# Performance work log

Measured on AMD Instinct MI355X. Metric: run time of the kernel, lower is better.

## Reference

```python
import jax, jax.numpy as jnp
import numpy as np

GRID_SIZE = 5
SPLINE_ORDER = 3
EPS = 1e-5


def make_grid(in_features):
    # efficient-kan: grid_range=[-1,1], points from -order..grid_size+order
    h = 2.0 / GRID_SIZE
    g = jnp.arange(-SPLINE_ORDER, GRID_SIZE + SPLINE_ORDER + 1, dtype=jnp.float32) * h - 1.0
    return jnp.tile(g[None, :], (in_features, 1))  # [in, grid_size + 2*order + 1]


def b_splines(x, grid):
    # x: [B, in], grid: [in, G] -> bases: [B, in, grid_size + order]
    xg = x[:, :, None]
    bases = ((xg >= grid[:, :-1]) & (xg < grid[:, 1:])).astype(x.dtype)
    for k in range(1, SPLINE_ORDER + 1):
        left = (xg - grid[:, : -(k + 1)]) / (grid[:, k:-1] - grid[:, : -(k + 1)])
        right = (grid[:, k + 1:] - xg) / (grid[:, k + 1:] - grid[:, 1:-k])
        bases = left * bases[:, :, :-1] + right * bases[:, :, 1:]
    return bases


def kan_linear(x, grid, base_w, spline_w, spline_scaler):
    # base path: silu(x) @ base_w.T ; spline path: bsplines(x) contracted with scaled spline weight
    base_out = jnp.einsum('bi,oi->bo', jax.nn.silu(x), base_w)
    bases = b_splines(x, grid)  # [B, in, C]
    sw = spline_w * spline_scaler[:, :, None]  # [out, in, C]
    spline_out = jnp.einsum('bic,oic->bo', bases, sw)
    return base_out + spline_out


def layer_norm(x, w, b):
    mu = jnp.mean(x, axis=-1, keepdims=True)
    var = jnp.mean(jnp.square(x - mu), axis=-1, keepdims=True)
    return (x - mu) * jax.lax.rsqrt(var + EPS) * w + b


def setup_inputs() -> dict:
    key = jax.random.key(0)
    ks = jax.random.split(key, 8)
    B, F, H, E = 65536, 32, 64, 64
    OUT = E * F  # 2048
    C = GRID_SIZE + SPLINE_ORDER  # 8 coeffs per edge
    x = jax.random.normal(ks[0], (B, F), dtype=jnp.float32)
    return {
        'x': x,
        'ln_w': jnp.ones((F,), jnp.float32),
        'ln_b': jnp.zeros((F,), jnp.float32),
        'bw1': jax.random.normal(ks[1], (H, F), jnp.float32) * 0.1,
        'sw1': jax.random.normal(ks[2], (H, F, C), jnp.float32) * 0.1,
        'ss1': jax.random.normal(ks[3], (H, F), jnp.float32) * 0.1 + 1.0,
        'bw2': jax.random.normal(ks[4], (OUT, H), jnp.float32) * 0.1,
        'sw2': jax.random.normal(ks[5], (OUT, H, C), jnp.float32) * 0.1,
        'ss2': jax.random.normal(ks[6], (OUT, H), jnp.float32) * 0.1 + 1.0,
        'grid1': make_grid(F),
        'grid2': make_grid(H),
    }


def reference(x, ln_w, ln_b, bw1, sw1, ss1, bw2, sw2, ss2, grid1, grid2):
    h = layer_norm(x, ln_w, ln_b)
    h = kan_linear(h, grid1, bw1, sw1, ss1)   # [B, 64]
    out = kan_linear(h, grid2, bw2, sw2, ss2)  # [B, 2048]
    return out
```

## Files before the change

### kernel.cpp

```cpp
#include <hip/hip_runtime.h>
#include <stdint.h>

#define BATCH   65536
#define FIN     32
#define HID     64
#define NOUT    2048
#define NC      8
#define NF      9
#define K1      288
#define K2      576

#define BM      256
#define BN      256
#define BK      32
#define KT      18
#define NBUF    4

typedef __bf16 bf16x8 __attribute__((ext_vector_type(8)));
typedef float f32x4 __attribute__((ext_vector_type(4)));

__device__ __forceinline__ uint16_t f2bf(float f) {
    uint32_t u = __builtin_bit_cast(uint32_t, f);
    uint32_t r = (u + 0x7fffu + ((u >> 16) & 1u)) >> 16;
    return (uint16_t)r;
}
__device__ __forceinline__ float silu_f(float v) {
    return v / (1.f + __expf(-v));
}

__device__ __forceinline__ void bspline8u(float xv, float out[8]) {
    float s = (xv + 2.2f) * 2.5f;
    int c = (int)floorf(s);
    float gc = (float)(c - 3) * 0.4f - 1.0f;
    float u = (xv - gc) * 2.5f;
    float u1 = 1.f - u;
    float uu = u * u, u3 = uu * u;
    float w0 = u1 * u1 * u1 * (1.f / 6.f);
    float w1 = (3.f * u3 - 6.f * uu + 4.f) * (1.f / 6.f);
    float w2 = (-3.f * u3 + 3.f * uu + 3.f * u + 1.f) * (1.f / 6.f);
    float w3 = u3 * (1.f / 6.f);
#pragma unroll
    for (int t = 0; t < 8; t++) {
        int d = c - t;
        out[t] = (d == 0) ? w3 : (d == 1) ? w2 : (d == 2) ? w1 : (d == 3) ? w0 : 0.f;
    }
}

__global__ void pack_w1(const float* __restrict__ bw1, const float* __restrict__ sw1,
                        const float* __restrict__ ss1, uint16_t* __restrict__ w1L) {
    int idx = blockIdx.x * 256 + threadIdx.x;
    if (idx >= 64 * K1) return;
    int o = idx / K1, k = idx % K1;
    int i = k / 9, j = k % 9;
    float v = (j == 0) ? bw1[o * FIN + i]
                       : sw1[(o * FIN + i) * NC + (j - 1)] * ss1[o * FIN + i];
    w1L[idx] = f2bf(v);
}

__global__ void pack_w2(const float* __restrict__ bw2, const float* __restrict__ sw2,
                        const float* __restrict__ ss2, uint16_t* __restrict__ w2p) {
    int idx = blockIdx.x * 256 + threadIdx.x;
    if (idx >= NOUT * K2) return;
    int n = idx / K2, k = idx % K2;
    int j = k >> 6, i = k & 63;
    float v = (j == 0) ? bw2[n * HID + i]
                       : sw2[(n * HID + i) * NC + (j - 1)] * ss2[n * HID + i];
    w2p[idx] = f2bf(v);
}

#define FBR   64
#define A1LD  296
__global__ __launch_bounds__(256) void featurize(
    const float* __restrict__ x, const float* __restrict__ lnw, const float* __restrict__ lnb,
    const uint16_t* __restrict__ w1L, uint16_t* __restrict__ a2) {

    __shared__ __align__(16) uint16_t w1s[64 * A1LD];
    __shared__ __align__(16) uint16_t a1s[FBR * A1LD];

    const int tid = threadIdx.x;
    const int wv = tid >> 6, lane = tid & 63;
    const int rowBase = blockIdx.x * FBR;

#pragma unroll
    for (int t = 0; t < 9; ++t) {
        int idx = t * 256 + tid;
        int o = idx / 36, cc = idx % 36;
        uint4 v = *(const uint4*)(w1L + idx * 8);
        *(uint4*)&w1s[o * A1LD + cc * 8] = v;
    }

    const int prow = tid >> 2, pq = tid & 3;
    const float* xp = x + (size_t)(rowBase + prow) * FIN + pq * 8;
    float xv[8];
    *(float4*)&xv[0] = ((const float4*)xp)[0];
    *(float4*)&xv[4] = ((const float4*)xp)[1];
    float s = 0.f, s2 = 0.f;
#pragma unroll
    for (int j = 0; j < 8; j++) { s += xv[j]; s2 += xv[j] * xv[j]; }
    s += __shfl_xor(s, 1);  s2 += __shfl_xor(s2, 1);
    s += __shfl_xor(s, 2);  s2 += __shfl_xor(s2, 2);
    const float mu = s * (1.f / 32.f);
    const float var = s2 * (1.f / 32.f) - mu * mu;
    const float rstd = rsqrtf(var + 1e-5f);

    float wl[8], bl[8];
    *(float4*)&wl[0] = ((const float4*)(lnw + pq * 8))[0];
    *(float4*)&wl[4] = ((const float4*)(lnw + pq * 8))[1];
    *(float4*)&bl[0] = ((const float4*)(lnb + pq * 8))[0];
    *(float4*)&bl[4] = ((const float4*)(lnb + pq * 8))[1];

    __align__(16) uint16_t tmp[72];
#pragma unroll
    for (int ii = 0; ii < 8; ii++) {
        float xn = (xv[ii] - mu) * rstd * wl[ii] + bl[ii];
        tmp[ii * 9] = f2bf(silu_f(xn));
        float bs[8];
        bspline8u(xn, bs);
#pragma unroll
        for (int j = 0; j < 8; j++) tmp[ii * 9 + 1 + j] = f2bf(bs[j]);
    }
    {
        uint16_t* dst = &a1s[prow * A1LD + pq * 72];
#pragma unroll
        for (int q = 0; q < 9; q++) *(uint4*)(dst + q * 8) = *(const uint4*)&tmp[q * 8];
    }
    __syncthreads();

    f32x4 acc[4];
#pragma unroll
    for (int n = 0; n < 4; n++) acc[n] = (f32x4){0.f, 0.f, 0.f, 0.f};
    const int arow = wv * 16 + (lane & 15);
    const int koff = (lane >> 4) * 8;
#pragma unroll
    for (int ks = 0; ks < 9; ++ks) {
        bf16x8 af = *(const bf16x8*)&a1s[arow * A1LD + ks * 32 + koff];
#pragma unroll
        for (int n = 0; n < 4; n++) {
            bf16x8 bv = *(const bf16x8*)&w1s[(n * 16 + (lane & 15)) * A1LD + ks * 32 + koff];
            acc[n] = __builtin_amdgcn_mfma_f32_16x16x32_bf16(af, bv, acc[n], 0, 0, 0);
        }
    }

    const int r0 = wv * 16 + ((lane >> 4) << 2);
    const int cb = lane & 15;
#pragma unroll
    for (int n = 0; n < 4; n++)
#pragma unroll
        for (int r = 0; r < 4; r++) {
            float h = acc[n][r];
            float o9[9];
            o9[0] = silu_f(h);
            bspline8u(h, &o9[1]);
            uint16_t* op = a2 + (size_t)(rowBase + r0 + r) * K2 + n * 16 + cb;
#pragma unroll
            for (int j = 0; j < 9; j++)
                __builtin_nontemporal_store(f2bf(o9[j]), op + j * 64);
        }
}

__device__ __forceinline__ void gload16(const uint16_t* g, const uint16_t* l) {
    __builtin_amdgcn_global_load_lds(
        (const __attribute__((address_space(1))) void*)g,
        (__attribute__((address_space(3))) void*)l, 16, 0, 0);
}

__global__ __launch_bounds__(512, 2) void gemm2_kernel(const uint16_t* __restrict__ A,
                                                       const uint16_t* __restrict__ Bt,
                                                       float* __restrict__ C) {
    __shared__ __align__(16) uint16_t lds[NBUF][2][BM * BK];

    const int tid = threadIdx.x;
    const int wv = tid >> 6, lane = tid & 63;
    const int wr = wv >> 2, wc = wv & 3;

    const uint32_t bid = blockIdx.x;
    const uint32_t wk = (bid & 7u) * 256u + (bid >> 3);
    const uint32_t ntile = wk & 7u, mtile = wk >> 3;

    const int srow = tid >> 2;
    const int scol = (((tid & 3) ^ ((tid >> 3) & 3)) << 3);
    const uint16_t* gA = A  + (size_t)(mtile * BM + srow) * K2 + scol;
    const uint16_t* gB = Bt + (size_t)(ntile * BN + srow) * K2 + scol;

#define STAGE_A(b, kt) do { \
    gload16(gA + (kt) * BK,                    &lds[b][0][wv * 512]); \
    gload16(gA + (size_t)128 * K2 + (kt) * BK, &lds[b][0][4096 + wv * 512]); } while (0)
#define STAGE_B(b, kt) do { \
    gload16(gB + (kt) * BK,                    &lds[b][1][wv * 512]); \
    gload16(gB + (size_t)128 * K2 + (kt) * BK, &lds[b][1][4096 + wv * 512]); } while (0)

    const int slot8 = (((lane >> 4) ^ ((lane >> 1) & 3)) << 3);
    const int aoff = (wr * 128 + (lane & 15)) * BK + slot8;
    const int boff = (wc * 64  + (lane & 15)) * BK + slot8;

    f32x4 acc[8][4];
#pragma unroll
    for (int m = 0; m < 8; m++)
#pragma unroll
        for (int n = 0; n < 4; n++) acc[m][n] = (f32x4){0.f, 0.f, 0.f, 0.f};

    STAGE_A(0, 0); STAGE_B(0, 0);
    STAGE_A(1, 1); STAGE_B(1, 1);
    STAGE_A(2, 2); STAGE_B(2, 2);
    asm volatile("s_waitcnt vmcnt(8)" ::: "memory");
    asm volatile("s_barrier" ::: "memory");

    for (int t = 0; t < KT; ++t) {
        const int b = t & 3;
        const uint16_t* As = &lds[b][0][0];
        const uint16_t* Bs = &lds[b][1][0];
        bf16x8 bv[4], af[4], ag[4];

#pragma unroll
        for (int n = 0; n < 4; ++n) bv[n] = *(const bf16x8*)&Bs[boff + n * 512];
#pragma unroll
        for (int m = 0; m < 4; ++m) af[m] = *(const bf16x8*)&As[aoff + m * 512];
        if (t < KT - 3) STAGE_A((t + 3) & 3, t + 3);
        __builtin_amdgcn_s_setprio(1);
#pragma unroll
        for (int m = 0; m < 4; ++m)
#pragma unroll
            for (int n = 0; n < 4; ++n)
                acc[m][n] = __builtin_amdgcn_mfma_f32_16x16x32_bf16(af[m], bv[n], acc[m][n], 0, 0, 0);
        __builtin_amdgcn_s_setprio(0);

#pragma unroll
        for (int m = 0; m < 4; ++m) ag[m] = *(const bf16x8*)&As[aoff + (m + 4) * 512];
        if (t < KT - 3) STAGE_B((t + 3) & 3, t + 3);
        __builtin_amdgcn_s_setprio(1);
#pragma unroll
        for (int m = 0; m < 4; ++m)
#pragma unroll
            for (int n = 0; n < 4; ++n)
                acc[m + 4][n] = __builtin_amdgcn_mfma_f32_16x16x32_bf16(ag[m], bv[n], acc[m + 4][n], 0, 0, 0);
        __builtin_amdgcn_s_setprio(0);

        if (t < KT - 3)       asm volatile("s_waitcnt vmcnt(8)" ::: "memory");
        else if (t == KT - 3) asm volatile("s_waitcnt vmcnt(4)" ::: "memory");
        else if (t <  KT - 1) asm volatile("s_waitcnt vmcnt(0)" ::: "memory");
        asm volatile("s_barrier" ::: "memory");
    }
#undef STAGE_A
#undef STAGE_B

    const int crow0 = (int)mtile * BM + wr * 128 + ((lane >> 4) << 2);
    const int ccol0 = (int)ntile * BN + wc * 64 + (lane & 15);
#pragma unroll
    for (int m = 0; m < 8; ++m)
#pragma unroll
        for (int n = 0; n < 4; ++n) {
            float* cp = C + (size_t)(crow0 + m * 16) * NOUT + ccol0 + n * 16;
#pragma unroll
            for (int r = 0; r < 4; ++r)
                __builtin_nontemporal_store(acc[m][n][r], cp + (size_t)r * NOUT);
        }
}

extern "C" void kernel_launch(void* const* d_in, const int* in_sizes, int n_in,
                              void* d_out, int out_size, void* d_ws, size_t ws_size,
                              hipStream_t stream) {
    const float* x    = (const float*)d_in[0];
    const float* lnw  = (const float*)d_in[1];
    const float* lnb  = (const float*)d_in[2];
    const float* bw1  = (const float*)d_in[3];
    const float* sw1  = (const float*)d_in[4];
    const float* ss1  = (const float*)d_in[5];
    const float* bw2  = (const float*)d_in[6];
    const float* sw2  = (const float*)d_in[7];
    const float* ss2  = (const float*)d_in[8];

    char* ws = (char*)d_ws;
    uint16_t* w1L = (uint16_t*)ws;
    uint16_t* w2p = (uint16_t*)(ws + 65536);
    uint16_t* a2  = (uint16_t*)(ws + 65536 + 2359296);
    float* out = (float*)d_out;

    pack_w1<<<dim3(72), dim3(256), 0, stream>>>(bw1, sw1, ss1, w1L);
    pack_w2<<<dim3((NOUT * K2 + 255) / 256), dim3(256), 0, stream>>>(bw2, sw2, ss2, w2p);
    featurize<<<dim3(BATCH / FBR), dim3(256), 0, stream>>>(x, lnw, lnb, w1L, a2);
    gemm2_kernel<<<dim3((BATCH / BM) * (NOUT / BN)), dim3(512), 0, stream>>>(a2, w2p, out);
}
```

Measured before the change: 348.2 us.

## Shrink GEMM tiles to 128x128 double-buffered and stage featurize output via LDS

```diff
diff --git a/kernel.cpp b/kernel.cpp
--- a/kernel.cpp
+++ b/kernel.cpp
@@ -10,11 +10,10 @@
 #define K1      288
 #define K2      576
 
-#define BM      256
-#define BN      256
-#define BK      32
-#define KT      18
-#define NBUF    4
+#define BM8     128
+#define BN8     128
+#define BK8     32
+#define KT8     18
 
 typedef __bf16 bf16x8 __attribute__((ext_vector_type(8)));
 typedef float f32x4 __attribute__((ext_vector_type(4)));
@@ -68,14 +67,17 @@
     w2p[idx] = f2bf(v);
 }
 
-#define FBR   64
-#define A1LD  296
+#define FBR    64
+#define A1LD   296
+#define S2LD   584
 __global__ __launch_bounds__(256) void featurize(
     const float* __restrict__ x, const float* __restrict__ lnw, const float* __restrict__ lnb,
     const uint16_t* __restrict__ w1L, uint16_t* __restrict__ a2) {
 
-    __shared__ __align__(16) uint16_t w1s[64 * A1LD];
-    __shared__ __align__(16) uint16_t a1s[FBR * A1LD];
+    __shared__ __align__(16) char fsm[75776];
+    uint16_t* w1s = (uint16_t*)fsm;
+    uint16_t* a1s = (uint16_t*)(fsm + 37888);
+    uint16_t* s2  = (uint16_t*)fsm;
 
     const int tid = threadIdx.x;
     const int wv = tid >> 6, lane = tid & 63;
@@ -94,13 +96,13 @@
     float xv[8];
     *(float4*)&xv[0] = ((const float4*)xp)[0];
     *(float4*)&xv[4] = ((const float4*)xp)[1];
-    float s = 0.f, s2 = 0.f;
-#pragma unroll
-    for (int j = 0; j < 8; j++) { s += xv[j]; s2 += xv[j] * xv[j]; }
-    s += __shfl_xor(s, 1);  s2 += __shfl_xor(s2, 1);
-    s += __shfl_xor(s, 2);  s2 += __shfl_xor(s2, 2);
+    float s = 0.f, s2v = 0.f;
+#pragma unroll
+    for (int j = 0; j < 8; j++) { s += xv[j]; s2v += xv[j] * xv[j]; }
+    s += __shfl_xor(s, 1);  s2v += __shfl_xor(s2v, 1);
+    s += __shfl_xor(s, 2);  s2v += __shfl_xor(s2v, 2);
     const float mu = s * (1.f / 32.f);
-    const float var = s2 * (1.f / 32.f) - mu * mu;
+    const float var = s2v * (1.f / 32.f) - mu * mu;
     const float rstd = rsqrtf(var + 1e-5f);
 
     float wl[8], bl[8];
@@ -140,6 +142,7 @@
             acc[n] = __builtin_amdgcn_mfma_f32_16x16x32_bf16(af, bv, acc[n], 0, 0, 0);
         }
     }
+    __syncthreads();
 
     const int r0 = wv * 16 + ((lane >> 4) << 2);
     const int cb = lane & 15;
@@ -151,11 +154,19 @@
             float o9[9];
             o9[0] = silu_f(h);
             bspline8u(h, &o9[1]);
-            uint16_t* op = a2 + (size_t)(rowBase + r0 + r) * K2 + n * 16 + cb;
-#pragma unroll
-            for (int j = 0; j < 9; j++)
-                __builtin_nontemporal_store(f2bf(o9[j]), op + j * 64);
+            uint16_t* op = &s2[(size_t)(r0 + r) * S2LD + n * 16 + cb];
+#pragma unroll
+            for (int j = 0; j < 9; j++) op[j * 64] = f2bf(o9[j]);
         }
+    __syncthreads();
+
+#pragma unroll
+    for (int q = 0; q < 18; ++q) {
+        int g = q * 256 + tid;
+        int row = g / 72, c = g % 72;
+        uint4 v = *(const uint4*)&s2[row * S2LD + c * 8];
+        *(uint4*)(a2 + (size_t)(rowBase + row) * K2 + c * 8) = v;
+    }
 }
 
 __device__ __forceinline__ void gload16(const uint16_t* g, const uint16_t* l) {
@@ -164,95 +175,73 @@
         (__attribute__((address_space(3))) void*)l, 16, 0, 0);
 }
 
-__global__ __launch_bounds__(512, 2) void gemm2_kernel(const uint16_t* __restrict__ A,
-                                                       const uint16_t* __restrict__ Bt,
-                                                       float* __restrict__ C) {
-    __shared__ __align__(16) uint16_t lds[NBUF][2][BM * BK];
+__global__ __launch_bounds__(256) void gemm2_kernel(const uint16_t* __restrict__ A,
+                                                    const uint16_t* __restrict__ Bt,
+                                                    float* __restrict__ C) {
+    __shared__ __align__(16) uint16_t As[2][BM8 * BK8];
+    __shared__ __align__(16) uint16_t Bs[2][BM8 * BK8];
 
     const int tid = threadIdx.x;
     const int wv = tid >> 6, lane = tid & 63;
-    const int wr = wv >> 2, wc = wv & 3;
+    const int wr = wv >> 1, wc = wv & 1;
 
     const uint32_t bid = blockIdx.x;
-    const uint32_t wk = (bid & 7u) * 256u + (bid >> 3);
-    const uint32_t ntile = wk & 7u, mtile = wk >> 3;
+    const uint32_t wk = (bid & 7u) * 1024u + (bid >> 3);
+    const uint32_t ntile = wk & 15u, mtile = wk >> 4;
 
     const int srow = tid >> 2;
-    const int scol = (((tid & 3) ^ ((tid >> 3) & 3)) << 3);
-    const uint16_t* gA = A  + (size_t)(mtile * BM + srow) * K2 + scol;
-    const uint16_t* gB = Bt + (size_t)(ntile * BN + srow) * K2 + scol;
-
-#define STAGE_A(b, kt) do { \
-    gload16(gA + (kt) * BK,                    &lds[b][0][wv * 512]); \
-    gload16(gA + (size_t)128 * K2 + (kt) * BK, &lds[b][0][4096 + wv * 512]); } while (0)
-#define STAGE_B(b, kt) do { \
-    gload16(gB + (kt) * BK,                    &lds[b][1][wv * 512]); \
-    gload16(gB + (size_t)128 * K2 + (kt) * BK, &lds[b][1][4096 + wv * 512]); } while (0)
-
-    const int slot8 = (((lane >> 4) ^ ((lane >> 1) & 3)) << 3);
-    const int aoff = (wr * 128 + (lane & 15)) * BK + slot8;
-    const int boff = (wc * 64  + (lane & 15)) * BK + slot8;
-
-    f32x4 acc[8][4];
-#pragma unroll
-    for (int m = 0; m < 8; m++)
+    const int scol = (((tid & 3) ^ (srow & 3)) << 3);
+    const uint16_t* gA = A  + (size_t)(mtile * BM8 + srow) * K2 + scol;
+    const uint16_t* gB = Bt + (size_t)(ntile * BN8 + srow) * K2 + scol;
+
+#define ST8(b, t) do { \
+    gload16(gA + (t) * BK8,                    &As[b][wv * 512]); \
+    gload16(gA + (size_t)64 * K2 + (t) * BK8,  &As[b][2048 + wv * 512]); \
+    gload16(gB + (t) * BK8,                    &Bs[b][wv * 512]); \
+    gload16(gB + (size_t)64 * K2 + (t) * BK8,  &Bs[b][2048 + wv * 512]); } while (0)
+
+    const int fswz = (((lane >> 4) ^ (lane & 3)) << 3);
+    const int aoff = (wr * 64 + (lane & 15)) * BK8 + fswz;
+    const int boff = (wc * 64 + (lane & 15)) * BK8 + fswz;
+
+    f32x4 acc[4][4];
+#pragma unroll
+    for (int m = 0; m < 4; m++)
 #pragma unroll
         for (int n = 0; n < 4; n++) acc[m][n] = (f32x4){0.f, 0.f, 0.f, 0.f};
 
-    STAGE_A(0, 0); STAGE_B(0, 0);
-    STAGE_A(1, 1); STAGE_B(1, 1);
-    STAGE_A(2, 2); STAGE_B(2, 2);
-    asm volatile("s_waitcnt vmcnt(8)" ::: "memory");
-    asm volatile("s_barrier" ::: "memory");
-
-    for (int t = 0; t < KT; ++t) {
-        const int b = t & 3;
-        const uint16_t* As = &lds[b][0][0];
-        const uint16_t* Bs = &lds[b][1][0];
-        bf16x8 bv[4], af[4], ag[4];
-
-#pragma unroll
-        for (int n = 0; n < 4; ++n) bv[n] = *(const bf16x8*)&Bs[boff + n * 512];
-#pragma unroll
-        for (int m = 0; m < 4; ++m) af[m] = *(const bf16x8*)&As[aoff + m * 512];
-        if (t < KT - 3) STAGE_A((t + 3) & 3, t + 3);
-        __builtin_amdgcn_s_setprio(1);
+    ST8(0, 0);
+    __syncthreads();
+
+#pragma unroll 2
+    for (int t = 0; t < KT8; ++t) {
+        const int b = t & 1;
+        if (t + 1 < KT8) ST8(b ^ 1, t + 1);
+
+        bf16x8 af[4], bv[4];
+#pragma unroll
+        for (int m = 0; m < 4; ++m) af[m] = *(const bf16x8*)&As[b][aoff + m * 16 * BK8];
+#pragma unroll
+        for (int n = 0; n < 4; ++n) bv[n] = *(const bf16x8*)&Bs[b][boff + n * 16 * BK8];
 #pragma unroll
         for (int m = 0; m < 4; ++m)
 #pragma unroll
             for (int n = 0; n < 4; ++n)
                 acc[m][n] = __builtin_amdgcn_mfma_f32_16x16x32_bf16(af[m], bv[n], acc[m][n], 0, 0, 0);
-        __builtin_amdgcn_s_setprio(0);
-
-#pragma unroll
-        for (int m = 0; m < 4; ++m) ag[m] = *(const bf16x8*)&As[aoff + (m + 4) * 512];
-        if (t < KT - 3) STAGE_B((t + 3) & 3, t + 3);
-        __builtin_amdgcn_s_setprio(1);
-#pragma unroll
-        for (int m = 0; m < 4; ++m)
-#pragma unroll
-            for (int n = 0; n < 4; ++n)
-                acc[m + 4][n] = __builtin_amdgcn_mfma_f32_16x16x32_bf16(ag[m], bv[n], acc[m + 4][n], 0, 0, 0);
-        __builtin_amdgcn_s_setprio(0);
-
-        if (t < KT - 3)       asm volatile("s_waitcnt vmcnt(8)" ::: "memory");
-        else if (t == KT - 3) asm volatile("s_waitcnt vmcnt(4)" ::: "memory");
-        else if (t <  KT - 1) asm volatile("s_waitcnt vmcnt(0)" ::: "memory");
-        asm volatile("s_barrier" ::: "memory");
-    }
-#undef STAGE_A
-#undef STAGE_B
-
-    const int crow0 = (int)mtile * BM + wr * 128 + ((lane >> 4) << 2);
-    const int ccol0 = (int)ntile * BN + wc * 64 + (lane & 15);
-#pragma unroll
-    for (int m = 0; m < 8; ++m)
+
+        __syncthreads();
+    }
+#undef ST8
+
+    const int crow0 = (int)mtile * BM8 + wr * 64 + ((lane >> 4) << 2);
+    const int ccol0 = (int)ntile * BN8 + wc * 64 + (lane & 15);
+#pragma unroll
+    for (int m = 0; m < 4; ++m)
 #pragma unroll
         for (int n = 0; n < 4; ++n) {
             float* cp = C + (size_t)(crow0 + m * 16) * NOUT + ccol0 + n * 16;
 #pragma unroll
-            for (int r = 0; r < 4; ++r)
-                __builtin_nontemporal_store(acc[m][n][r], cp + (size_t)r * NOUT);
+            for (int r = 0; r < 4; ++r) cp[(size_t)r * NOUT] = acc[m][n][r];
         }
 }
 
@@ -278,5 +267,5 @@
     pack_w1<<<dim3(72), dim3(256), 0, stream>>>(bw1, sw1, ss1, w1L);
     pack_w2<<<dim3((NOUT * K2 + 255) / 256), dim3(256), 0, stream>>>(bw2, sw2, ss2, w2p);
     featurize<<<dim3(BATCH / FBR), dim3(256), 0, stream>>>(x, lnw, lnb, w1L, a2);
-    gemm2_kernel<<<dim3((BATCH / BM) * (NOUT / BN)), dim3(512), 0, stream>>>(a2, w2p, out);
-}
+    gemm2_kernel<<<dim3((BATCH / BM8) * (NOUT / BN8)), dim3(256), 0, stream>>>(a2, w2p, out);
+}
```

Result: no change. 341.4 us (-1.9%).
